# Performance work log

Hardware: AMD Instinct MI355X
Metric: run time of the kernel (lower is better)

## Reference

```python
import jax, jax.numpy as jnp
import numpy as np

B, L, LQ = 64, 4096, 128
D = 32        # input_dim (value channels)
ET = 128      # embed_time
NH = 1        # num_heads
H = 128       # nhidden
NC = 6        # n_classes


def _time_emb(tt, lin_w, lin_b, per_w, per_b):
    # tt [..., T] -> [..., T, ET]; cat(Linear(1,1)(t), sin(Linear(1,ET-1)(t)))
    tt = tt[..., None]
    out1 = tt * lin_w[0, 0] + lin_b
    out2 = jnp.sin(tt @ per_w + per_b)
    return jnp.concatenate([out1, out2], axis=-1)


def _gru_dir(xs, wih, whh, bih, bhh, reverse):
    # xs [B, T, I] -> [B, T, H]; torch GRU gate math
    xs_t = jnp.swapaxes(xs, 0, 1)              # [T, B, I]
    if reverse:
        xs_t = xs_t[::-1]
    gi_all = xs_t @ wih.T + bih                # [T, B, 3H] precomputed input gates
    h0 = jnp.zeros((xs.shape[0], H), xs.dtype)

    def step(h, gi):
        gh = h @ whh.T + bhh
        ir, iz, inn = jnp.split(gi, 3, axis=-1)
        hr, hz, hn = jnp.split(gh, 3, axis=-1)
        r = jax.nn.sigmoid(ir + hr)
        z = jax.nn.sigmoid(iz + hz)
        n = jnp.tanh(inn + r * hn)
        h_new = (1.0 - z) * n + z * h
        return h_new, h_new

    _, ys = jax.lax.scan(step, h0, gi_all)     # [T, B, H]
    if reverse:
        ys = ys[::-1]
    return jnp.swapaxes(ys, 0, 1)


def _bigru(xs, wih, whh, bih, bhh):
    fwd = _gru_dir(xs, wih[0], whh[0], bih[0], bhh[0], False)
    bwd = _gru_dir(xs, wih[1], whh[1], bih[1], bhh[1], True)
    return jnp.concatenate([fwd, bwd], axis=-1)


def setup_inputs() -> dict:
    ks = jax.random.split(jax.random.key(0), 32)
    w = lambda i, s: jax.random.normal(ks[i], s, jnp.float32) * 0.05
    G3 = 3 * H
    return {
        "x": jax.random.normal(ks[0], (B, L, D), jnp.float32),
        "time_steps": jax.random.uniform(ks[1], (B, L), dtype=jnp.float32),
        "query_times": jnp.linspace(0.0, 1.0, LQ, dtype=jnp.float32),
        "lin_w": w(2, (1, 1)), "lin_b": w(3, (1,)),
        "per_w": w(4, (1, ET - 1)), "per_b": w(5, (ET - 1,)),
        "wq": w(6, (ET, ET)), "bq": w(7, (ET,)),
        "wk": w(8, (ET, ET)), "bk": w(9, (ET,)),
        "wo": w(10, (NH * D, H)), "bo": w(11, (H,)),
        "gru0_wih": w(12, (2, G3, H)), "gru0_whh": w(13, (2, G3, H)),
        "gru0_bih": w(14, (2, G3)), "gru0_bhh": w(15, (2, G3)),
        "gru1_wih": w(16, (2, G3, 2 * H)), "gru1_whh": w(17, (2, G3, H)),
        "gru1_bih": w(18, (2, G3)), "gru1_bhh": w(19, (2, G3)),
        "c1_w": w(20, (2 * H, 128)), "c1_b": w(21, (128,)),
        "c2_w": w(22, (128, 64)), "c2_b": w(23, (64,)),
        "c3_w": w(24, (64, NC)), "c3_b": w(25, (NC,)),
    }


def reference(x, time_steps, query_times, lin_w, lin_b, per_w, per_b,
              wq, bq, wk, bk, wo, bo,
              gru0_wih, gru0_whh, gru0_bih, gru0_bhh,
              gru1_wih, gru1_whh, gru1_bih, gru1_bhh,
              c1_w, c1_b, c2_w, c2_b, c3_w, c3_b):
    ek = ET // NH
    # learned time embeddings
    q = _time_emb(query_times[None, :], lin_w, lin_b, per_w, per_b)  # [1, LQ, ET]
    k = _time_emb(time_steps, lin_w, lin_b, per_w, per_b)            # [B, L, ET]
    # per-head projections
    qp = (q @ wq + bq).reshape(1, LQ, NH, ek).transpose(0, 2, 1, 3)[0]  # [NH, LQ, ek]
    kp = (k @ wk + bk).reshape(B, L, NH, ek).transpose(0, 2, 1, 3)      # [B, NH, L, ek]
    # mTAN attention: scores are channel-independent (mask=None), so the
    # per-channel repeat+softmax reduces to a single softmax over keys.
    scores = jnp.einsum('hqe,bhke->bhqk', qp, kp) / jnp.sqrt(jnp.float32(ek))
    p = jax.nn.softmax(scores, axis=-1)                                 # [B, NH, LQ, L]
    att = jnp.einsum('bhqk,bkd->bqhd', p, x).reshape(B, LQ, NH * D)
    att_out = att @ wo + bo                                             # [B, LQ, H]
    # 2-layer bidirectional GRU
    g0 = _bigru(att_out, gru0_wih, gru0_whh, gru0_bih, gru0_bhh)        # [B, LQ, 2H]
    g1 = _bigru(g0, gru1_wih, gru1_whh, gru1_bih, gru1_bhh)             # [B, LQ, 2H]
    class_in = jnp.concatenate([g1[:, -1, :H], g1[:, 0, H:]], axis=1)   # [B, 2H]
    out = ((class_in @ c1_w + c1_b) @ c2_w + c2_b) @ c3_w + c3_b        # [B, NC]
    return out
```

## Files before the change

kernel.cpp:

```cpp
#include <hip/hip_runtime.h>
#include <math.h>

#define Bn   64
#define Ln   4096
#define LQn  128
#define Dn   32
#define ETn  128
#define Hn   128
#define G3n  384
#define NDEG 12

typedef __attribute__((ext_vector_type(2))) float f32x2;
typedef __attribute__((ext_vector_type(2))) _Float16 f16x2;
typedef __attribute__((ext_vector_type(8))) _Float16 f16x8;
typedef __attribute__((ext_vector_type(4))) float f32x4;

#define DPPF(x, ctrl) __int_as_float(__builtin_amdgcn_update_dpp(0, __float_as_int(x), (ctrl), 0xF, 0xF, true))
#define QP_XOR1 0xB1
#define QP_XOR2 0x4E
#define QP_B0   0x00
#define QP_B1   0x55
#define QP_B2   0xAA
#define QP_B3   0xFF

__device__ __forceinline__ float sin_poly(float x) {
    const float x2 = x * x;
    float r = -1.9841270114e-04f;
    r = fmaf(r, x2,  8.3333337680e-03f);
    r = fmaf(r, x2, -1.6666667163e-01f);
    return fmaf(r * x2, x, x);
}
__device__ __forceinline__ float cos_poly(float x) {
    const float x2 = x * x;
    float r =  2.4801587642e-05f;
    r = fmaf(r, x2, -1.3888888899e-03f);
    r = fmaf(r, x2,  4.1666667908e-02f);
    r = fmaf(r, x2, -5.0000000000e-01f);
    return fmaf(r, x2, 1.0f);
}

#define WS_C    0
#define WS_WT   4096
#define WS_B2   (WS_WT + 768*32)
#define WS_CLS  (WS_B2 + 1024)
#define WS_G0   (WS_CLS + Bn*2*Hn)
#define WS_GI   (WS_G0 + Bn*LQn*2*Hn)
#define WS_ACCP WS_G0
#define WS_SP   WS_CLS
#define WS_W16  (WS_G0 + 1100000)

__global__ __launch_bounds__(128) void k_coef(
    const float* __restrict__ qtimes, const float* __restrict__ lin_w,
    const float* __restrict__ lin_b, const float* __restrict__ per_w,
    const float* __restrict__ per_b, const float* __restrict__ wq,
    const float* __restrict__ bq, const float* __restrict__ wk,
    const float* __restrict__ bk, float* __restrict__ C)
{
    __shared__ float qe[ETn], qp_l[ETn], qt_l[ETn], bas[NDEG * 128], red[96], qbk_red[32];
    const int q = blockIdx.x, tid = threadIdx.x;
    if (tid < ETn - 1) {
        const float w = per_w[tid], bb = per_b[tid];
        const float sb = sin_poly(bb), cb = cos_poly(bb);
        float wp = 1.f;
#pragma unroll
        for (int d = 0; d < NDEG; ++d) {
            const float sd = ((d & 3) == 0) ? sb : ((d & 3) == 1) ? cb : ((d & 3) == 2) ? -sb : -cb;
            bas[d * 128 + tid] = wp * sd;
            wp *= w / (float)(d + 1);
        }
    }
    const float t = qtimes[q];
    qe[tid] = (tid == 0) ? fmaf(t, lin_w[0], lin_b[0])
                         : sin_poly(fmaf(t, per_w[tid - 1], per_b[tid - 1]));
    __syncthreads();
    {
        float a = bq[tid];
#pragma unroll 16
        for (int i = 0; i < ETn; ++i) a = fmaf(qe[i], wq[i * ETn + tid], a);
        qp_l[tid] = a;
    }
    __syncthreads();
    {
        const float4* wk4 = (const float4*)(wk + (size_t)tid * ETn);
        const float4* qp4 = (const float4*)qp_l;
        float a = 0.f;
#pragma unroll
        for (int k = 0; k < 32; ++k) {
            const float4 w4 = wk4[k], p4 = qp4[k];
            a += w4.x * p4.x + w4.y * p4.y + w4.z * p4.z + w4.w * p4.w;
        }
        qt_l[tid] = a;
    }
    __syncthreads();
    if (tid < 96) {
        const int d = tid >> 3, g = tid & 7;
        float p = 0.f;
        for (int j = g; j < ETn - 1; j += 8) p = fmaf(qt_l[j + 1], bas[d * 128 + j], p);
        red[tid] = p;
    } else {
        const int g2 = tid - 96;
        float p = 0.f;
#pragma unroll
        for (int k = 0; k < 4; ++k) p = fmaf(qp_l[g2 + 32 * k], bk[g2 + 32 * k], p);
        qbk_red[g2] = p;
    }
    __syncthreads();
    if (tid < NDEG) {
        const int d = tid;
        float s = red[d * 8 + 0] + red[d * 8 + 1] + red[d * 8 + 2] + red[d * 8 + 3]
                + red[d * 8 + 4] + red[d * 8 + 5] + red[d * 8 + 6] + red[d * 8 + 7];
        if (d == 0) {
            float qbk = 0.f;
#pragma unroll
            for (int k = 0; k < 32; ++k) qbk += qbk_red[k];
            s += qt_l[0] * lin_b[0] + qbk;
        }
        if (d == 1) s += qt_l[0] * lin_w[0];
        C[q * NDEG + d] = s * 0.08838834764831845f;
    }
}

__global__ __launch_bounds__(256) void k_fuse(
    const float* __restrict__ wih, const float* __restrict__ wo,
    const float* __restrict__ bo, const float* __restrict__ bih,
    float* __restrict__ Wt, float* __restrict__ bias2, float* __restrict__ sP)
{
    const int t = blockIdx.x * 256 + threadIdx.x;
    if (t < 768 * 32) {
        const int o = t >> 5, d = t & 31;
        const float4* wr4 = (const float4*)(wih + (size_t)o * 128);
        const float4* wc4 = (const float4*)(wo + (size_t)d * 128);
        float a = 0.f;
#pragma unroll
        for (int k = 0; k < 32; ++k) {
            const float4 r4 = wr4[k], c4 = wc4[k];
            a += r4.x * c4.x + r4.y * c4.y + r4.z * c4.z + r4.w * c4.w;
        }
        Wt[t] = a;
    } else if (t < 768 * 33) {
        const int o = t - 768 * 32;
        const float4* wr4 = (const float4*)(wih + (size_t)o * 128);
        const float4* bo4 = (const float4*)bo;
        float a = bih[o];
#pragma unroll
        for (int k = 0; k < 32; ++k) {
            const float4 r4 = wr4[k], b4 = bo4[k];
            a += r4.x * b4.x + r4.y * b4.y + r4.z * b4.z + r4.w * b4.w;
        }
        bias2[o] = a;
    } else if (t < 768 * 33 + Bn * LQn) {
        sP[t - 768 * 33] = 0.f;
    }
}

__global__ __launch_bounds__(256) void k_w16(
    const float* __restrict__ w, _Float16* __restrict__ w16)
{
    const int idx = blockIdx.x * 256 + threadIdx.x;
    if (idx < 768 * 256) w16[idx] = (_Float16)w[idx];
}

__global__ __launch_bounds__(512, 4) void k_attn(
    const float* __restrict__ x, const float* __restrict__ tsteps,
    const float* __restrict__ Cc, float* __restrict__ accP, float* __restrict__ sP)
{
    __shared__ __align__(16) char smem[4 * 128 * 36 * 4];
    float4* xls  = (float4*)smem;
    float*  slabf = (float*)smem;
#define SLAB(s, qq, c) slabf[(((s) * 128) + (qq)) * 36 + (c)]
    const int tid = threadIdx.x;
    const int b = blockIdx.x >> 3, lsplit = blockIdx.x & 7;
    const int i = tid & 3, qt = (tid >> 2) & 31, ls2 = tid >> 7;
    const int qown = 4 * qt + i;
    const int u = tid & 127;

    float c[NDEG];
#pragma unroll
    for (int d = 0; d < NDEG; ++d) c[d] = Cc[qown * NDEG + d];

    const int l0 = lsplit * 512 + ls2 * 128;
    const float4* tg4 = (const float4*)(tsteps + (size_t)b * Ln + l0);
    const float4* xg  = (const float4*)(x + ((size_t)b * Ln + l0) * Dn);

    f32x2 acc2[4][4];
#pragma unroll
    for (int m = 0; m < 4; ++m)
#pragma unroll
        for (int e = 0; e < 4; ++e) { acc2[m][e].x = 0.f; acc2[m][e].y = 0.f; }
    float s_own = 0.f;

    float4 xr[4];
#pragma unroll
    for (int w = 0; w < 4; ++w) xr[w] = xg[u + 128 * w];

    for (int ch = 0; ch < 2; ++ch) {
        __syncthreads();
#pragma unroll
        for (int w = 0; w < 4; ++w) xls[ls2 * 512 + u + 128 * w] = xr[w];
        __syncthreads();
        if (ch < 1) {
            const int off = 512;
#pragma unroll
            for (int w = 0; w < 4; ++w) xr[w] = xg[off + u + 128 * w];
        }
        const float4* xrow = &xls[ls2 * 512];
        for (int k = 0; k < 16; ++k) {
            const float4 t4 = tg4[ch * 16 + k];
#pragma unroll
            for (int jj = 0; jj < 4; ++jj) {
                const float t = (jj == 0) ? t4.x : (jj == 1) ? t4.y : (jj == 2) ? t4.z : t4.w;
                float sc = c[NDEG - 1];
#pragma unroll
                for (int d = NDEG - 2; d >= 0; --d) sc = fmaf(sc, t, c[d]);
                const float pe = __expf(sc);
                s_own += pe;
                const float p0 = DPPF(pe, QP_B0);
                const float p1 = DPPF(pe, QP_B1);
                const float p2 = DPPF(pe, QP_B2);
                const float p3 = DPPF(pe, QP_B3);
                const int lrow = (k * 4 + jj) * 8;
                const float4 xa = xrow[lrow + 2 * i];
                const float4 xb = xrow[lrow + 2 * i + 1];
                f32x2 xa0; xa0.x = xa.x; xa0.y = xa.y;
                f32x2 xa1; xa1.x = xa.z; xa1.y = xa.w;
                f32x2 xb0; xb0.x = xb.x; xb0.y = xb.y;
                f32x2 xb1; xb1.x = xb.z; xb1.y = xb.w;
#define PKA(m, pv) { f32x2 pp; pp.x = (pv); pp.y = (pv); \
    acc2[m][0] = __builtin_elementwise_fma(pp, xa0, acc2[m][0]); \
    acc2[m][1] = __builtin_elementwise_fma(pp, xa1, acc2[m][1]); \
    acc2[m][2] = __builtin_elementwise_fma(pp, xb0, acc2[m][2]); \
    acc2[m][3] = __builtin_elementwise_fma(pp, xb1, acc2[m][3]); }
                PKA(0, p0) PKA(1, p1) PKA(2, p2) PKA(3, p3)
#undef PKA
            }
        }
    }
    __syncthreads();
#pragma unroll
    for (int m = 0; m < 4; ++m) {
        float4 f4a, f4b;
        f4a.x = acc2[m][0].x; f4a.y = acc2[m][0].y; f4a.z = acc2[m][1].x; f4a.w = acc2[m][1].y;
        f4b.x = acc2[m][2].x; f4b.y = acc2[m][2].y; f4b.z = acc2[m][3].x; f4b.w = acc2[m][3].y;
        *(float4*)&SLAB(ls2, 4 * qt + m, 8 * i)     = f4a;
        *(float4*)&SLAB(ls2, 4 * qt + m, 8 * i + 4) = f4b;
    }
    SLAB(ls2, qown, 32) = s_own;
    __syncthreads();
    const int q = tid & 127, part = tid >> 7;
#pragma unroll
    for (int j = 0; j < 2; ++j) {
        const int off = (part * 2 + j) * 4;
        float4 r  = *(float4*)&SLAB(0, q, off);
        float4 r1 = *(float4*)&SLAB(1, q, off);
        float4 r2 = *(float4*)&SLAB(2, q, off);
        float4 r3 = *(float4*)&SLAB(3, q, off);
        r.x += r1.x + r2.x + r3.x; r.y += r1.y + r2.y + r3.y;
        r.z += r1.z + r2.z + r3.z; r.w += r1.w + r2.w + r3.w;
        *(float4*)&accP[((((size_t)lsplit * Bn + b) * LQn + q) * 32) + off] = r;
    }
    if (part == 0) {
        atomicAdd(&sP[(size_t)b * LQn + q],
                  SLAB(0, q, 32) + SLAB(1, q, 32) + SLAB(2, q, 32) + SLAB(3, q, 32));
    }
#undef SLAB
}

__global__ __launch_bounds__(256) void k_gemm_att(
    const float* __restrict__ accP, const float* __restrict__ sP,
    const float* __restrict__ Bm, const float* __restrict__ bias,
    float* __restrict__ Cm)
{
    __shared__ float4 A_l[64 * 8];
    __shared__ float4 B_l[64 * 8];
    const int tid = threadIdx.x;
    const int m0 = blockIdx.x * 64, n0 = blockIdx.y * 64;
    const int r0 = (tid >> 4) << 2, c0 = (tid & 15) << 2;
    f32x2 acc2[4][4];
#pragma unroll
    for (int a = 0; a < 4; ++a)
#pragma unroll
        for (int bb = 0; bb < 4; ++bb) { acc2[a][bb].x = 0.f; acc2[a][bb].y = 0.f; }
    const float4* Ag = (const float4*)accP;
    const float4* Bg = (const float4*)Bm;

#pragma unroll
    for (int w = 0; w < 2; ++w) {
        const int idx = tid + w * 256;
        const int row = idx >> 3, c4 = idx & 7;
        const int sc = (c4 + row + (row >> 2)) & 7;
        const int m = m0 + row;
        float4 av = Ag[(size_t)m * 8 + c4];
#pragma unroll
        for (int s = 1; s < 8; ++s) {
            const float4 as = Ag[((size_t)s * 8192 + m) * 8 + c4];
            av.x += as.x; av.y += as.y; av.z += as.z; av.w += as.w;
        }
        const float inv = 1.f / sP[m];
        av.x *= inv; av.y *= inv; av.z *= inv; av.w *= inv;
        A_l[row * 8 + sc] = av;
        B_l[row * 8 + sc] = Bg[(size_t)(n0 + row) * 8 + c4];
    }
    __syncthreads();
#pragma unroll
    for (int k4 = 0; k4 < 8; ++k4) {
        float4 av[4], bv[4];
#pragma unroll
        for (int j = 0; j < 4; ++j) {
            const int ra = r0 + j;
            av[j] = A_l[ra * 8 + ((k4 + ra + (ra >> 2)) & 7)];
        }
#pragma unroll
        for (int j = 0; j < 4; ++j) {
            const int rb = c0 + j;
            bv[j] = B_l[rb * 8 + ((k4 + rb + (rb >> 2)) & 7)];
        }
#pragma unroll
        for (int ri = 0; ri < 4; ++ri) {
            f32x2 alo; alo.x = av[ri].x; alo.y = av[ri].y;
            f32x2 ahi; ahi.x = av[ri].z; ahi.y = av[ri].w;
#pragma unroll
            for (int ci = 0; ci < 4; ++ci) {
                f32x2 blo; blo.x = bv[ci].x; blo.y = bv[ci].y;
                f32x2 bhi; bhi.x = bv[ci].z; bhi.y = bv[ci].w;
                acc2[ri][ci] = __builtin_elementwise_fma(alo, blo, acc2[ri][ci]);
                acc2[ri][ci] = __builtin_elementwise_fma(ahi, bhi, acc2[ri][ci]);
            }
        }
    }
#pragma unroll
    for (int ri = 0; ri < 4; ++ri) {
        float4 o4;
        o4.x = acc2[ri][0].x + acc2[ri][0].y + bias[n0 + c0 + 0];
        o4.y = acc2[ri][1].x + acc2[ri][1].y + bias[n0 + c0 + 1];
        o4.z = acc2[ri][2].x + acc2[ri][2].y + bias[n0 + c0 + 2];
        o4.w = acc2[ri][3].x + acc2[ri][3].y + bias[n0 + c0 + 3];
        *(float4*)&Cm[(size_t)(m0 + r0 + ri) * 768 + n0 + c0] = o4;
    }
}

__global__ __launch_bounds__(256) void k_gemm16(
    const _Float16* __restrict__ g0, const _Float16* __restrict__ w16,
    const float* __restrict__ bias, float* __restrict__ Cm)
{
    const int tid = threadIdx.x;
    const int wave = tid >> 6, lane = tid & 63;
    const int m0 = blockIdx.x * 64 + wave * 16;
    const int n0 = blockIdx.y * 64;
    const int koff = 8 * (lane >> 4);

    const _Float16* Ab  = g0 + (size_t)(m0 + (lane & 15)) * 256 + koff;
    const _Float16* Bb0 = w16 + (size_t)(n0 +  0 + (lane & 15)) * 256 + koff;
    const _Float16* Bb1 = w16 + (size_t)(n0 + 16 + (lane & 15)) * 256 + koff;
    const _Float16* Bb2 = w16 + (size_t)(n0 + 32 + (lane & 15)) * 256 + koff;
    const _Float16* Bb3 = w16 + (size_t)(n0 + 48 + (lane & 15)) * 256 + koff;

    f32x4 acc0 = {0.f, 0.f, 0.f, 0.f}, acc1 = acc0, acc2 = acc0, acc3 = acc0;
#pragma unroll
    for (int k0 = 0; k0 < 256; k0 += 32) {
        const f16x8 a  = *(const f16x8*)(Ab  + k0);
        const f16x8 b0 = *(const f16x8*)(Bb0 + k0);
        const f16x8 b1 = *(const f16x8*)(Bb1 + k0);
        const f16x8 b2 = *(const f16x8*)(Bb2 + k0);
        const f16x8 b3 = *(const f16x8*)(Bb3 + k0);
        acc0 = __builtin_amdgcn_mfma_f32_16x16x32_f16(a, b0, acc0, 0, 0, 0);
        acc1 = __builtin_amdgcn_mfma_f32_16x16x32_f16(a, b1, acc1, 0, 0, 0);
        acc2 = __builtin_amdgcn_mfma_f32_16x16x32_f16(a, b2, acc2, 0, 0, 0);
        acc3 = __builtin_amdgcn_mfma_f32_16x16x32_f16(a, b3, acc3, 0, 0, 0);
    }
    const int mr = m0 + (lane >> 4) * 4;
    const int nc = lane & 15;
#pragma unroll
    for (int r = 0; r < 4; ++r) {
        Cm[(size_t)(mr + r) * 768 + n0 +  0 + nc] = acc0[r] + bias[n0 +  0 + nc];
        Cm[(size_t)(mr + r) * 768 + n0 + 16 + nc] = acc1[r] + bias[n0 + 16 + nc];
        Cm[(size_t)(mr + r) * 768 + n0 + 32 + nc] = acc2[r] + bias[n0 + 32 + nc];
        Cm[(size_t)(mr + r) * 768 + n0 + 48 + nc] = acc3[r] + bias[n0 + 48 + nc];
    }
}

__global__ __launch_bounds__(256, 1) void k_gru(
    const float* __restrict__ gi, const float* __restrict__ whh,
    const float* __restrict__ bhh, _Float16* __restrict__ seq_out,
    float* __restrict__ final_out)
{
    __shared__ _Float16 h16[2][Hn];
    __shared__ float    h32[2][Hn];
    const int tid = threadIdx.x;
    const int b = blockIdx.x >> 1, dir = blockIdx.x & 1;
    const int j = tid >> 1, q = tid & 1;

    f16x2 wr[32], wz[32], wn[32];
    {
        const float* wb = whh + ((size_t)dir * G3n + j) * Hn + 64 * q;
        const f32x2* p0 = (const f32x2*)(wb);
        const f32x2* p1 = (const f32x2*)(wb + (size_t)128 * Hn);
        const f32x2* p2 = (const f32x2*)(wb + (size_t)256 * Hn);
#pragma unroll
        for (int k = 0; k < 32; ++k) {
            f32x2 a = p0[k], z2 = p1[k], c2 = p2[k];
            wr[k].x = (_Float16)a.x;  wr[k].y = (_Float16)a.y;
            wz[k].x = (_Float16)z2.x; wz[k].y = (_Float16)z2.y;
            wn[k].x = (_Float16)c2.x; wn[k].y = (_Float16)c2.y;
        }
    }
#pragma unroll
    for (int k = 0; k < 32; ++k) {
        asm volatile("" : "+v"(wr[k]));
        asm volatile("" : "+v"(wz[k]));
        asm volatile("" : "+v"(wn[k]));
    }
    const float bhr = bhh[dir * G3n + j];
    const float bhz = bhh[dir * G3n + 128 + j];
    const float bhn = bhh[dir * G3n + 256 + j];

    if (tid < Hn) {
        h32[0][tid] = 0.f; h32[1][tid] = 0.f;
        h16[0][tid] = (_Float16)0.f; h16[1][tid] = (_Float16)0.f;
    }
    __syncthreads();

    const long sstride = dir ? -768 : 768;
    const float* gptr = gi + (size_t)b * LQn * 768 + dir * G3n + j
                        + (size_t)(dir ? LQn - 1 : 0) * 768;

    int cur = 0;
    float hlast = 0.f;

    auto gstep = [&](const float gir, const float giz, const float gin, const int step) {
        const float hold = h32[cur][j];
        const float4* hb4 = (const float4*)(&h16[cur][64 * q]);
        float srA = 0.f, szA = 0.f, snA = 0.f;
        float srB = 0.f, szB = 0.f, snB = 0.f;
#pragma unroll
        for (int k2 = 0; k2 < 4; ++k2) {
            float4 hv = hb4[k2];
            f16x2 h0 = *(f16x2*)&hv.x;
            f16x2 h1 = *(f16x2*)&hv.y;
            f16x2 h2 = *(f16x2*)&hv.z;
            f16x2 h3 = *(f16x2*)&hv.w;
            asm("v_dot2_f32_f16 %0, %1, %2, %0" : "+v"(srA) : "v"(wr[4 * k2 + 0]), "v"(h0));
            asm("v_dot2_f32_f16 %0, %1, %2, %0" : "+v"(szA) : "v"(wz[4 * k2 + 0]), "v"(h0));
            asm("v_dot2_f32_f16 %0, %1, %2, %0" : "+v"(snA) : "v"(wn[4 * k2 + 0]), "v"(h0));
            asm("v_dot2_f32_f16 %0, %1, %2, %0" : "+v"(srA) : "v"(wr[4 * k2 + 1]), "v"(h1));
            asm("v_dot2_f32_f16 %0, %1, %2, %0" : "+v"(szA) : "v"(wz[4 * k2 + 1]), "v"(h1));
            asm("v_dot2_f32_f16 %0, %1, %2, %0" : "+v"(snA) : "v"(wn[4 * k2 + 1]), "v"(h1));
            asm("v_dot2_f32_f16 %0, %1, %2, %0" : "+v"(srA) : "v"(wr[4 * k2 + 2]), "v"(h2));
            asm("v_dot2_f32_f16 %0, %1, %2, %0" : "+v"(szA) : "v"(wz[4 * k2 + 2]), "v"(h2));
            asm("v_dot2_f32_f16 %0, %1, %2, %0" : "+v"(snA) : "v"(wn[4 * k2 + 2]), "v"(h2));
            asm("v_dot2_f32_f16 %0, %1, %2, %0" : "+v"(srA) : "v"(wr[4 * k2 + 3]), "v"(h3));
            asm("v_dot2_f32_f16 %0, %1, %2, %0" : "+v"(szA) : "v"(wz[4 * k2 + 3]), "v"(h3));
            asm("v_dot2_f32_f16 %0, %1, %2, %0" : "+v"(snA) : "v"(wn[4 * k2 + 3]), "v"(h3));
        }
#pragma unroll
        for (int k2 = 4; k2 < 8; ++k2) {
            float4 hv = hb4[k2];
            f16x2 h0 = *(f16x2*)&hv.x;
            f16x2 h1 = *(f16x2*)&hv.y;
            f16x2 h2 = *(f16x2*)&hv.z;
            f16x2 h3 = *(f16x2*)&hv.w;
            asm("v_dot2_f32_f16 %0, %1, %2, %0" : "+v"(srB) : "v"(wr[4 * k2 + 0]), "v"(h0));
            asm("v_dot2_f32_f16 %0, %1, %2, %0" : "+v"(szB) : "v"(wz[4 * k2 + 0]), "v"(h0));
            asm("v_dot2_f32_f16 %0, %1, %2, %0" : "+v"(snB) : "v"(wn[4 * k2 + 0]), "v"(h0));
            asm("v_dot2_f32_f16 %0, %1, %2, %0" : "+v"(srB) : "v"(wr[4 * k2 + 1]), "v"(h1));
            asm("v_dot2_f32_f16 %0, %1, %2, %0" : "+v"(szB) : "v"(wz[4 * k2 + 1]), "v"(h1));
            asm("v_dot2_f32_f16 %0, %1, %2, %0" : "+v"(snB) : "v"(wn[4 * k2 + 1]), "v"(h1));
            asm("v_dot2_f32_f16 %0, %1, %2, %0" : "+v"(srB) : "v"(wr[4 * k2 + 2]), "v"(h2));
            asm("v_dot2_f32_f16 %0, %1, %2, %0" : "+v"(szB) : "v"(wz[4 * k2 + 2]), "v"(h2));
            asm("v_dot2_f32_f16 %0, %1, %2, %0" : "+v"(snB) : "v"(wn[4 * k2 + 2]), "v"(h2));
            asm("v_dot2_f32_f16 %0, %1, %2, %0" : "+v"(srB) : "v"(wr[4 * k2 + 3]), "v"(h3));
            asm("v_dot2_f32_f16 %0, %1, %2, %0" : "+v"(szB) : "v"(wz[4 * k2 + 3]), "v"(h3));
            asm("v_dot2_f32_f16 %0, %1, %2, %0" : "+v"(snB) : "v"(wn[4 * k2 + 3]), "v"(h3));
        }
        float sr = srA + srB, sz = szA + szB, sn = snA + snB;
        sr += DPPF(sr, QP_XOR1);
        sz += DPPF(sz, QP_XOR1);
        sn += DPPF(sn, QP_XOR1);
        const float r = 1.f / (1.f + __expf(-(gir + sr + bhr)));
        const float z = 1.f / (1.f + __expf(-(giz + sz + bhz)));
        const float nx = gin + r * (sn + bhn);
        const float n = 1.f - 2.f / (1.f + __expf(2.f * nx));
        const float hn = n + z * (hold - n);
        if (q == 0) {
            h32[cur ^ 1][j] = hn;
            h16[cur ^ 1][j] = (_Float16)hn;
            if (seq_out) {
                const int l = dir ? (LQn - 1 - step) : step;
                seq_out[((size_t)(b * LQn + l)) * (2 * Hn) + dir * Hn + j] = (_Float16)hn;
            }
        }
        hlast = hn;
        cur ^= 1;
        asm volatile("s_waitcnt lgkmcnt(0)\n\ts_barrier" ::: "memory");
    };

    float gA[3], gB[3];
#define GLD(dst, s) { const long o = (long)(s) * sstride; \
    dst[0] = gptr[o]; dst[1] = gptr[o + 128]; dst[2] = gptr[o + 256]; }
    GLD(gA, 0) GLD(gB, 1)
    for (int s0 = 0; s0 < LQn; s0 += 2) {
        gstep(gA[0], gA[1], gA[2], s0);
        { const int sn2 = (s0 + 2 < LQn) ? s0 + 2 : LQn - 1; GLD(gA, sn2) }
        gstep(gB[0], gB[1], gB[2], s0 + 1);
        { const int sn2 = (s0 + 3 < LQn) ? s0 + 3 : LQn - 1; GLD(gB, sn2) }
    }
#undef GLD
    if (final_out && q == 0) final_out[b * 2 * Hn + dir * Hn + j] = hlast;
}

__global__ __launch_bounds__(256) void k_cls(
    const float* __restrict__ cls_in,
    const float* __restrict__ c1w, const float* __restrict__ c1b,
    const float* __restrict__ c2w, const float* __restrict__ c2b,
    const float* __restrict__ c3w, const float* __restrict__ c3b,
    float* __restrict__ out)
{
    __shared__ float ci[256], y1[128], y2[64];
    const int b = blockIdx.x, tid = threadIdx.x;
    ci[tid] = cls_in[b * 256 + tid];
    __syncthreads();
    if (tid < 128) { float a = c1b[tid]; for (int i = 0; i < 256; ++i) a += ci[i] * c1w[i * 128 + tid]; y1[tid] = a; }
    __syncthreads();
    if (tid < 64)  { float a = c2b[tid]; for (int i = 0; i < 128; ++i) a += y1[i] * c2w[i * 64 + tid];  y2[tid] = a; }
    __syncthreads();
    if (tid < 6)   { float a = c3b[tid]; for (int i = 0; i < 64; ++i)  a += y2[i] * c3w[i * 6 + tid];   out[b * 6 + tid] = a; }
}

extern "C" void kernel_launch(void* const* d_in, const int* in_sizes, int n_in,
                              void* d_out, int out_size, void* d_ws, size_t ws_size,
                              hipStream_t stream)
{
    const float* x        = (const float*)d_in[0];
    const float* tsteps   = (const float*)d_in[1];
    const float* qtimes   = (const float*)d_in[2];
    const float* lin_w    = (const float*)d_in[3];
    const float* lin_b    = (const float*)d_in[4];
    const float* per_w    = (const float*)d_in[5];
    const float* per_b    = (const float*)d_in[6];
    const float* wq       = (const float*)d_in[7];
    const float* bq       = (const float*)d_in[8];
    const float* wk       = (const float*)d_in[9];
    const float* bk       = (const float*)d_in[10];
    const float* wo       = (const float*)d_in[11];
    const float* bo       = (const float*)d_in[12];
    const float* g0_wih   = (const float*)d_in[13];
    const float* g0_whh   = (const float*)d_in[14];
    const float* g0_bih   = (const float*)d_in[15];
    const float* g0_bhh   = (const float*)d_in[16];
    const float* g1_wih   = (const float*)d_in[17];
    const float* g1_whh   = (const float*)d_in[18];
    const float* g1_bih   = (const float*)d_in[19];
    const float* g1_bhh   = (const float*)d_in[20];
    const float* c1w      = (const float*)d_in[21];
    const float* c1b      = (const float*)d_in[22];
    const float* c2w      = (const float*)d_in[23];
    const float* c2b      = (const float*)d_in[24];
    const float* c3w      = (const float*)d_in[25];
    const float* c3b      = (const float*)d_in[26];
    float* out = (float*)d_out;
    float* ws  = (float*)d_ws;

    float* Cws   = ws + WS_C;
    float* Wt    = ws + WS_WT;
    float* bias2 = ws + WS_B2;
    float* clsin = ws + WS_CLS;
    float* accP  = ws + WS_ACCP;
    float* sPb   = ws + WS_SP;
    float* gibuf = ws + WS_GI;
    _Float16* g0f16 = (_Float16*)(ws + WS_G0);
    _Float16* w16b  = (_Float16*)(ws + WS_W16);

    k_coef<<<128, 128, 0, stream>>>(qtimes, lin_w, lin_b, per_w, per_b, wq, bq, wk, bk, Cws);
    k_fuse<<<131, 256, 0, stream>>>(g0_wih, wo, bo, g0_bih, Wt, bias2, sPb);
    k_attn<<<512, 512, 0, stream>>>(x, tsteps, Cws, accP, sPb);

    k_gemm_att<<<dim3(128, 12), 256, 0, stream>>>(accP, sPb, Wt, bias2, gibuf);
    k_w16<<<768, 256, 0, stream>>>(g1_wih, w16b);
    k_gru<<<128, 256, 0, stream>>>(gibuf, g0_whh, g0_bhh, g0f16, nullptr);

    k_gemm16<<<dim3(128, 12), 256, 0, stream>>>(g0f16, w16b, g1_bih, gibuf);
    k_gru<<<128, 256, 0, stream>>>(gibuf, g1_whh, g1_bhh, nullptr, clsin);

    k_cls<<<64, 256, 0, stream>>>(clsin, c1w, c1b, c2w, c2b, c3w, c3b, out);
}
```

Measured before the change: 270.9 us.

## Split GRU hidden-unit dot products across 8 lanes with 1024-thread blocks

```diff
diff --git a/kernel.cpp b/kernel.cpp
--- a/kernel.cpp
+++ b/kernel.cpp
@@ -22,6 +22,7 @@
 #define QP_B1   0x55
 #define QP_B2   0xAA
 #define QP_B3   0xFF
+#define ROW_HALF_MIRROR 0x141
 
 __device__ __forceinline__ float sin_poly(float x) {
     const float x2 = x * x;
@@ -378,7 +379,7 @@
     }
 }
 
-__global__ __launch_bounds__(256, 1) void k_gru(
+__global__ __launch_bounds__(1024, 4) void k_gru(
     const float* __restrict__ gi, const float* __restrict__ whh,
     const float* __restrict__ bhh, _Float16* __restrict__ seq_out,
     float* __restrict__ final_out)
@@ -387,16 +388,16 @@
     __shared__ float    h32[2][Hn];
     const int tid = threadIdx.x;
     const int b = blockIdx.x >> 1, dir = blockIdx.x & 1;
-    const int j = tid >> 1, q = tid & 1;
-
-    f16x2 wr[32], wz[32], wn[32];
+    const int j = tid >> 3, q = tid & 7;
+
+    f16x2 wr[8], wz[8], wn[8];
     {
-        const float* wb = whh + ((size_t)dir * G3n + j) * Hn + 64 * q;
+        const float* wb = whh + ((size_t)dir * G3n + j) * Hn + 16 * q;
         const f32x2* p0 = (const f32x2*)(wb);
         const f32x2* p1 = (const f32x2*)(wb + (size_t)128 * Hn);
         const f32x2* p2 = (const f32x2*)(wb + (size_t)256 * Hn);
 #pragma unroll
-        for (int k = 0; k < 32; ++k) {
+        for (int k = 0; k < 8; ++k) {
             f32x2 a = p0[k], z2 = p1[k], c2 = p2[k];
             wr[k].x = (_Float16)a.x;  wr[k].y = (_Float16)a.y;
             wz[k].x = (_Float16)z2.x; wz[k].y = (_Float16)z2.y;
@@ -404,7 +405,7 @@
         }
     }
 #pragma unroll
-    for (int k = 0; k < 32; ++k) {
+    for (int k = 0; k < 8; ++k) {
         asm volatile("" : "+v"(wr[k]));
         asm volatile("" : "+v"(wz[k]));
         asm volatile("" : "+v"(wn[k]));
@@ -413,68 +414,49 @@
     const float bhz = bhh[dir * G3n + 128 + j];
     const float bhn = bhh[dir * G3n + 256 + j];
 
-    if (tid < Hn) {
-        h32[0][tid] = 0.f; h32[1][tid] = 0.f;
-        h16[0][tid] = (_Float16)0.f; h16[1][tid] = (_Float16)0.f;
+    if (tid < 2 * Hn) {
+        ((float*)h32)[tid] = 0.f;
+        ((_Float16*)h16)[tid] = (_Float16)0.f;
     }
     __syncthreads();
 
     const long sstride = dir ? -768 : 768;
-    const float* gptr = gi + (size_t)b * LQn * 768 + dir * G3n + j
-                        + (size_t)(dir ? LQn - 1 : 0) * 768;
+    const float* gib = gi + ((size_t)b * LQn + (size_t)(dir ? LQn - 1 : 0)) * 768
+                       + dir * G3n + j;
 
     int cur = 0;
     float hlast = 0.f;
 
-    auto gstep = [&](const float gir, const float giz, const float gin, const int step) {
+    auto gstep = [&](const float gv, const int step) {
         const float hold = h32[cur][j];
-        const float4* hb4 = (const float4*)(&h16[cur][64 * q]);
-        float srA = 0.f, szA = 0.f, snA = 0.f;
-        float srB = 0.f, szB = 0.f, snB = 0.f;
-#pragma unroll
-        for (int k2 = 0; k2 < 4; ++k2) {
-            float4 hv = hb4[k2];
+        const float4* hb = (const float4*)(&h16[cur][16 * q]);
+        float sr = 0.f, sz = 0.f, sn = 0.f;
+#pragma unroll
+        for (int k2 = 0; k2 < 2; ++k2) {
+            const float4 hv = hb[k2];
             f16x2 h0 = *(f16x2*)&hv.x;
             f16x2 h1 = *(f16x2*)&hv.y;
             f16x2 h2 = *(f16x2*)&hv.z;
             f16x2 h3 = *(f16x2*)&hv.w;
-            asm("v_dot2_f32_f16 %0, %1, %2, %0" : "+v"(srA) : "v"(wr[4 * k2 + 0]), "v"(h0));
-            asm("v_dot2_f32_f16 %0, %1, %2, %0" : "+v"(szA) : "v"(wz[4 * k2 + 0]), "v"(h0));
-            asm("v_dot2_f32_f16 %0, %1, %2, %0" : "+v"(snA) : "v"(wn[4 * k2 + 0]), "v"(h0));
-            asm("v_dot2_f32_f16 %0, %1, %2, %0" : "+v"(srA) : "v"(wr[4 * k2 + 1]), "v"(h1));
-            asm("v_dot2_f32_f16 %0, %1, %2, %0" : "+v"(szA) : "v"(wz[4 * k2 + 1]), "v"(h1));
-            asm("v_dot2_f32_f16 %0, %1, %2, %0" : "+v"(snA) : "v"(wn[4 * k2 + 1]), "v"(h1));
-            asm("v_dot2_f32_f16 %0, %1, %2, %0" : "+v"(srA) : "v"(wr[4 * k2 + 2]), "v"(h2));
-            asm("v_dot2_f32_f16 %0, %1, %2, %0" : "+v"(szA) : "v"(wz[4 * k2 + 2]), "v"(h2));
-            asm("v_dot2_f32_f16 %0, %1, %2, %0" : "+v"(snA) : "v"(wn[4 * k2 + 2]), "v"(h2));
-            asm("v_dot2_f32_f16 %0, %1, %2, %0" : "+v"(srA) : "v"(wr[4 * k2 + 3]), "v"(h3));
-            asm("v_dot2_f32_f16 %0, %1, %2, %0" : "+v"(szA) : "v"(wz[4 * k2 + 3]), "v"(h3));
-            asm("v_dot2_f32_f16 %0, %1, %2, %0" : "+v"(snA) : "v"(wn[4 * k2 + 3]), "v"(h3));
-        }
-#pragma unroll
-        for (int k2 = 4; k2 < 8; ++k2) {
-            float4 hv = hb4[k2];
-            f16x2 h0 = *(f16x2*)&hv.x;
-            f16x2 h1 = *(f16x2*)&hv.y;
-            f16x2 h2 = *(f16x2*)&hv.z;
-            f16x2 h3 = *(f16x2*)&hv.w;
-            asm("v_dot2_f32_f16 %0, %1, %2, %0" : "+v"(srB) : "v"(wr[4 * k2 + 0]), "v"(h0));
-            asm("v_dot2_f32_f16 %0, %1, %2, %0" : "+v"(szB) : "v"(wz[4 * k2 + 0]), "v"(h0));
-            asm("v_dot2_f32_f16 %0, %1, %2, %0" : "+v"(snB) : "v"(wn[4 * k2 + 0]), "v"(h0));
-            asm("v_dot2_f32_f16 %0, %1, %2, %0" : "+v"(srB) : "v"(wr[4 * k2 + 1]), "v"(h1));
-            asm("v_dot2_f32_f16 %0, %1, %2, %0" : "+v"(szB) : "v"(wz[4 * k2 + 1]), "v"(h1));
-            asm("v_dot2_f32_f16 %0, %1, %2, %0" : "+v"(snB) : "v"(wn[4 * k2 + 1]), "v"(h1));
-            asm("v_dot2_f32_f16 %0, %1, %2, %0" : "+v"(srB) : "v"(wr[4 * k2 + 2]), "v"(h2));
-            asm("v_dot2_f32_f16 %0, %1, %2, %0" : "+v"(szB) : "v"(wz[4 * k2 + 2]), "v"(h2));
-            asm("v_dot2_f32_f16 %0, %1, %2, %0" : "+v"(snB) : "v"(wn[4 * k2 + 2]), "v"(h2));
-            asm("v_dot2_f32_f16 %0, %1, %2, %0" : "+v"(srB) : "v"(wr[4 * k2 + 3]), "v"(h3));
-            asm("v_dot2_f32_f16 %0, %1, %2, %0" : "+v"(szB) : "v"(wz[4 * k2 + 3]), "v"(h3));
-            asm("v_dot2_f32_f16 %0, %1, %2, %0" : "+v"(snB) : "v"(wn[4 * k2 + 3]), "v"(h3));
-        }
-        float sr = srA + srB, sz = szA + szB, sn = snA + snB;
-        sr += DPPF(sr, QP_XOR1);
-        sz += DPPF(sz, QP_XOR1);
-        sn += DPPF(sn, QP_XOR1);
+            asm("v_dot2_f32_f16 %0, %1, %2, %0" : "+v"(sr) : "v"(wr[4 * k2 + 0]), "v"(h0));
+            asm("v_dot2_f32_f16 %0, %1, %2, %0" : "+v"(sz) : "v"(wz[4 * k2 + 0]), "v"(h0));
+            asm("v_dot2_f32_f16 %0, %1, %2, %0" : "+v"(sn) : "v"(wn[4 * k2 + 0]), "v"(h0));
+            asm("v_dot2_f32_f16 %0, %1, %2, %0" : "+v"(sr) : "v"(wr[4 * k2 + 1]), "v"(h1));
+            asm("v_dot2_f32_f16 %0, %1, %2, %0" : "+v"(sz) : "v"(wz[4 * k2 + 1]), "v"(h1));
+            asm("v_dot2_f32_f16 %0, %1, %2, %0" : "+v"(sn) : "v"(wn[4 * k2 + 1]), "v"(h1));
+            asm("v_dot2_f32_f16 %0, %1, %2, %0" : "+v"(sr) : "v"(wr[4 * k2 + 2]), "v"(h2));
+            asm("v_dot2_f32_f16 %0, %1, %2, %0" : "+v"(sz) : "v"(wz[4 * k2 + 2]), "v"(h2));
+            asm("v_dot2_f32_f16 %0, %1, %2, %0" : "+v"(sn) : "v"(wn[4 * k2 + 2]), "v"(h2));
+            asm("v_dot2_f32_f16 %0, %1, %2, %0" : "+v"(sr) : "v"(wr[4 * k2 + 3]), "v"(h3));
+            asm("v_dot2_f32_f16 %0, %1, %2, %0" : "+v"(sz) : "v"(wz[4 * k2 + 3]), "v"(h3));
+            asm("v_dot2_f32_f16 %0, %1, %2, %0" : "+v"(sn) : "v"(wn[4 * k2 + 3]), "v"(h3));
+        }
+        sr += DPPF(sr, QP_XOR1); sr += DPPF(sr, QP_XOR2); sr += DPPF(sr, ROW_HALF_MIRROR);
+        sz += DPPF(sz, QP_XOR1); sz += DPPF(sz, QP_XOR2); sz += DPPF(sz, ROW_HALF_MIRROR);
+        sn += DPPF(sn, QP_XOR1); sn += DPPF(sn, QP_XOR2); sn += DPPF(sn, ROW_HALF_MIRROR);
+        const float gir = DPPF(gv, QP_B0);
+        const float giz = DPPF(gv, QP_B1);
+        const float gin = DPPF(gv, QP_B2);
         const float r = 1.f / (1.f + __expf(-(gir + sr + bhr)));
         const float z = 1.f / (1.f + __expf(-(giz + sz + bhz)));
         const float nx = gin + r * (sn + bhn);
@@ -493,14 +475,14 @@
         asm volatile("s_waitcnt lgkmcnt(0)\n\ts_barrier" ::: "memory");
     };
 
-    float gA[3], gB[3];
-#define GLD(dst, s) { const long o = (long)(s) * sstride; \
-    dst[0] = gptr[o]; dst[1] = gptr[o + 128]; dst[2] = gptr[o + 256]; }
-    GLD(gA, 0) GLD(gB, 1)
+    float gA, gB;
+#define GLD(d, s) { d = (q < 3) ? gib[(long)(s) * sstride + q * Hn] : 0.f; }
+    GLD(gA, 0)
+    GLD(gB, 1)
     for (int s0 = 0; s0 < LQn; s0 += 2) {
-        gstep(gA[0], gA[1], gA[2], s0);
+        gstep(gA, s0);
         { const int sn2 = (s0 + 2 < LQn) ? s0 + 2 : LQn - 1; GLD(gA, sn2) }
-        gstep(gB[0], gB[1], gB[2], s0 + 1);
+        gstep(gB, s0 + 1);
         { const int sn2 = (s0 + 3 < LQn) ? s0 + 3 : LQn - 1; GLD(gB, sn2) }
     }
 #undef GLD
@@ -575,10 +557,10 @@
 
     k_gemm_att<<<dim3(128, 12), 256, 0, stream>>>(accP, sPb, Wt, bias2, gibuf);
     k_w16<<<768, 256, 0, stream>>>(g1_wih, w16b);
-    k_gru<<<128, 256, 0, stream>>>(gibuf, g0_whh, g0_bhh, g0f16, nullptr);
+    k_gru<<<128, 1024, 0, stream>>>(gibuf, g0_whh, g0_bhh, g0f16, nullptr);
 
     k_gemm16<<<dim3(128, 12), 256, 0, stream>>>(g0f16, w16b, g1_bih, gibuf);
-    k_gru<<<128, 256, 0, stream>>>(gibuf, g1_whh, g1_bhh, nullptr, clsin);
+    k_gru<<<128, 1024, 0, stream>>>(gibuf, g1_whh, g1_bhh, nullptr, clsin);
 
     k_cls<<<64, 256, 0, stream>>>(clsin, c1w, c1b, c2w, c2b, c3w, c3b, out);
 }
```

Measured after the change: 350.7 us. 29.4% more time.
